# Optimization experiments

Measured on AMD Instinct MI355X. Metric: run time of the kernel, lower is better.

The kernel has to match this reference:

```python
import jax, jax.numpy as jnp
import numpy as np

N, E, G, F = 100000, 3200000, 256, 15
NEG_SLOPE = 0.2


def _lin(k, fi, fo):
    s = 1.0 / np.sqrt(fi)
    return jax.random.uniform(k, (fi, fo), jnp.float32, -s, s)


def _vec(k, n, fi):
    s = 1.0 / np.sqrt(fi)
    return jax.random.uniform(k, (n,), jnp.float32, -s, s)


def setup_inputs() -> dict:
    key = jax.random.key(0)
    ks = jax.random.split(key, 40)
    inp = {}
    inp["x"] = jax.random.normal(ks[0], (N, F), jnp.float32)
    inp["edge_index"] = jax.random.randint(ks[1], (2, E), 0, N, dtype=jnp.int32)
    inp["batch"] = jnp.sort(jax.random.randint(ks[2], (N,), 0, G, dtype=jnp.int32))
    inp["xA"] = jax.random.normal(ks[3], (G, 300), jnp.float32)
    i = 4
    for l in (1, 2, 3):
        inp[f"cW{l}"] = _lin(ks[i], F, F); i += 1
        inp[f"cas{l}"] = _vec(ks[i], F, F); i += 1
        inp[f"cad{l}"] = _vec(ks[i], F, F); i += 1
        inp[f"cb{l}"] = jnp.zeros((F,), jnp.float32)
        inp[f"fW{l}"] = _lin(ks[i], F, F); i += 1
        inp[f"fb{l}"] = _vec(ks[i], F, F); i += 1
    inp["m1W"] = _lin(ks[i], 90, 90); i += 1
    inp["m1b"] = _vec(ks[i], 90, 90); i += 1
    inp["aW1"] = _lin(ks[i], 300, 300); i += 1
    inp["ab1"] = _vec(ks[i], 300, 300); i += 1
    inp["aW2"] = _lin(ks[i], 300, 300); i += 1
    inp["ab2"] = _vec(ks[i], 300, 300); i += 1
    inp["aW3"] = _lin(ks[i], 300, 300); i += 1
    inp["ab3"] = _vec(ks[i], 300, 300); i += 1
    inp["aW4"] = _lin(ks[i], 300, 45); i += 1
    inp["ab4"] = _vec(ks[i], 45, 300); i += 1
    inp["m2W"] = _lin(ks[i], 90, 1); i += 1
    inp["m2b"] = _vec(ks[i], 1, 90); i += 1
    return inp


def _gat(x, src, dst, W, a_s, a_d, b):
    """PyG GATConv (heads=1, add_self_loops handled by caller via src/dst)."""
    h = x @ W                                        # [N, F]
    e = jax.nn.leaky_relu((h @ a_s)[src] + (h @ a_d)[dst], NEG_SLOPE)  # [E+N]
    mx = jax.ops.segment_max(e, dst, num_segments=N)
    ex = jnp.exp(e - mx[dst])
    den = jax.ops.segment_sum(ex, dst, num_segments=N)
    alpha = ex / (den[dst] + 1e-16)                   # segment softmax over dst
    out = jax.ops.segment_sum(h[src] * alpha[:, None], dst, num_segments=N)
    return out + b


def reference(x, edge_index, batch, xA,
              cW1, cas1, cad1, cb1, fW1, fb1,
              cW2, cas2, cad2, cb2, fW2, fb2,
              cW3, cas3, cad3, cb3, fW3, fb3,
              m1W, m1b, aW1, ab1, aW2, ab2, aW3, ab3, aW4, ab4,
              m2W, m2b):
    loop = jnp.arange(N, dtype=edge_index.dtype)      # self loops
    src = jnp.concatenate([edge_index[0], loop])
    dst = jnp.concatenate([edge_index[1], loop])

    h = _gat(x, src, dst, cW1, cas1, cad1, cb1)
    h = jax.nn.relu(h @ fW1 + fb1)
    h = _gat(h, src, dst, cW2, cas2, cad2, cb2)
    h = jax.nn.relu(h @ fW2 + fb2)
    h = _gat(h, src, dst, cW3, cas3, cad3, cb3)
    h = h @ fW3 + fb3

    s = jax.ops.segment_sum(h, batch, num_segments=G)
    mx = jax.ops.segment_max(h, batch, num_segments=G)
    cnt = jax.ops.segment_sum(jnp.ones((N, 1), h.dtype), batch, num_segments=G)
    mean = s / jnp.maximum(cnt, 1.0)
    pooled = jnp.concatenate([s, mx, mean], axis=1)   # [G, 45]

    a = jax.nn.relu(xA @ aW1 + ab1)
    a = jax.nn.relu(a @ aW2 + ab2)
    a = jax.nn.sigmoid(a @ aW3 + ab3)
    xann = a @ aW4 + ab4                              # [G, 45]

    z = jnp.concatenate([pooled, xann], axis=1)       # [G, 90]
    z = jax.nn.relu(z @ m1W + m1b)
    z = z @ m2W + m2b
    return jax.nn.sigmoid(z)
```

## Files before the change

### kernel.cpp

```cpp
#include <hip/hip_runtime.h>
#include <hip/hip_bf16.h>
#include <math.h>

#define FDIM 15
#define FPAD 16
#define NEG_SLOPE 0.2f
#define BSH 8
#define BWID 256
#define HB_GRID 256
#define HB_BLK 1024

typedef _Float16 half_t;

__device__ __forceinline__ float leaky(float e) {
  return fmaxf(NEG_SLOPE * e, e);
}

__global__ void k_zero(int* __restrict__ p, int n) {
  int i = blockIdx.x * blockDim.x + threadIdx.x;
  if (i < n) p[i] = 0;
}

__global__ void k_bhist(const int* __restrict__ dstI, int* __restrict__ bcnt,
                        int n_tot, int n_real, int NB) {
  __shared__ int hist[512];
  int tid = threadIdx.x;
  for (int i = tid; i < NB; i += blockDim.x) hist[i] = 0;
  __syncthreads();
  int stride = gridDim.x * blockDim.x;
  for (int i = blockIdx.x * blockDim.x + tid; i < n_tot; i += stride) {
    int d = (i < n_real) ? dstI[i] : (i - n_real);
    atomicAdd(&hist[d >> BSH], 1);
  }
  __syncthreads();
  for (int i = tid; i < NB; i += blockDim.x)
    if (hist[i]) atomicAdd(&bcnt[i], hist[i]);
}

__global__ void k_bscan(const int* __restrict__ bcnt, int* __restrict__ boff,
                        int* __restrict__ bcur, int* __restrict__ rowptr,
                        int NB, int N, int total) {
  __shared__ int s[512];
  int tid = threadIdx.x;
  int v = (tid < NB) ? bcnt[tid] : 0;
  s[tid] = v;
  __syncthreads();
  for (int off = 1; off < 512; off <<= 1) {
    int add = (tid >= off) ? s[tid - off] : 0;
    __syncthreads();
    s[tid] += add;
    __syncthreads();
  }
  if (tid < NB) { int e = s[tid] - v; boff[tid] = e; bcur[tid] = e; }
  if (tid == NB - 1) boff[NB] = s[tid];
  if (tid == 0) rowptr[N] = total;
}

__global__ void k_bpart(const int* __restrict__ srcI, const int* __restrict__ dstI,
                        int* __restrict__ bcur, int* __restrict__ bbuf,
                        int n_tot, int n_real, int NB) {
  __shared__ int hist[512];
  __shared__ int base[512];
  int tid = threadIdx.x;
  for (int i = tid; i < NB; i += blockDim.x) hist[i] = 0;
  __syncthreads();
  int stride = gridDim.x * blockDim.x;
  int g0 = blockIdx.x * blockDim.x + tid;
  for (int i = g0; i < n_tot; i += stride) {
    int d = (i < n_real) ? dstI[i] : (i - n_real);
    atomicAdd(&hist[d >> BSH], 1);
  }
  __syncthreads();
  for (int i = tid; i < NB; i += blockDim.x)
    base[i] = hist[i] ? atomicAdd(&bcur[i], hist[i]) : 0;
  __syncthreads();
  for (int i = tid; i < NB; i += blockDim.x) hist[i] = 0;
  __syncthreads();
  for (int i = g0; i < n_tot; i += stride) {
    int s, d;
    if (i < n_real) { s = srcI[i]; d = dstI[i]; }
    else { s = d = i - n_real; }
    int b = d >> BSH;
    int p = base[b] + atomicAdd(&hist[b], 1);
    bbuf[p] = (s << BSH) | (d & (BWID - 1));
  }
}

__global__ void k_bbuild(const int* __restrict__ boff, const int* __restrict__ bbuf,
                         int* __restrict__ rowptr, int* __restrict__ csr, int N) {
  __shared__ int hist[BWID];
  __shared__ int sc[BWID];
  int b = blockIdx.x;
  int tid = threadIdx.x;
  int base_dst = b << BSH;
  int nd = min(BWID, N - base_dst);
  int s0 = boff[b], s1 = boff[b + 1];
  if (tid < BWID) hist[tid] = 0;
  __syncthreads();
  for (int j = s0 + tid; j < s1; j += 512)
    atomicAdd(&hist[bbuf[j] & (BWID - 1)], 1);
  __syncthreads();
  int v = 0;
  if (tid < BWID) { v = hist[tid]; sc[tid] = v; }
  __syncthreads();
  for (int off = 1; off < BWID; off <<= 1) {
    int add = 0;
    if (tid < BWID && tid >= off) add = sc[tid - off];
    __syncthreads();
    if (tid < BWID) sc[tid] += add;
    __syncthreads();
  }
  if (tid < nd) rowptr[base_dst + tid] = s0 + sc[tid] - v;
  __syncthreads();
  if (tid < BWID) hist[tid] = sc[tid] - v;
  __syncthreads();
  for (int j = s0 + tid; j < s1; j += 512) {
    int e = bbuf[j];
    int dl = e & (BWID - 1);
    int p = s0 + atomicAdd(&hist[dl], 1);
    csr[p] = (e >> BSH) << 5;
  }
}

__global__ void k_transform(const float* __restrict__ in, int ld_in,
                            const float* __restrict__ W,
                            const float* __restrict__ a_s,
                            const float* __restrict__ a_d,
                            half_t* __restrict__ hp,
                            float* __restrict__ ad_,
                            int n_nodes) {
  __shared__ float Ws[FDIM * FDIM];
  __shared__ float asv[FDIM], adv[FDIM];
  int tid = threadIdx.x;
  if (tid < FDIM * FDIM) Ws[tid] = W[tid];
  if (tid < FDIM) { asv[tid] = a_s[tid]; adv[tid] = a_d[tid]; }
  __syncthreads();
  int n = blockIdx.x * blockDim.x + tid;
  if (n >= n_nodes) return;
  float xin[FDIM];
#pragma unroll
  for (int j = 0; j < FDIM; ++j) xin[j] = in[n * ld_in + j];
  float sa = 0.f, da = 0.f;
  half_t hrow[FPAD];
#pragma unroll
  for (int o = 0; o < FDIM; ++o) {
    float acc = 0.f;
#pragma unroll
    for (int k = 0; k < FDIM; ++k) acc += xin[k] * Ws[k * FDIM + o];
    hrow[o] = (half_t)acc;
    sa += acc * asv[o];
    da += acc * adv[o];
  }
  hrow[FDIM] = (half_t)sa;
  ad_[n] = da;
  float4 w0, w1;
  __builtin_memcpy(&w0, &hrow[0], 16);
  __builtin_memcpy(&w1, &hrow[8], 16);
  float4* dst = (float4*)(hp + (size_t)n * FPAD);
  dst[0] = w0;
  dst[1] = w1;
}

__device__ __forceinline__ void mlp_rider(int g, int tid, int nthreads,
                                          const float* __restrict__ mIn,
                                          const float* __restrict__ mW,
                                          const float* __restrict__ mB,
                                          float* __restrict__ mOut,
                                          int Nout, int mAct,
                                          float* mins) {
  for (int k = tid; k < 300; k += nthreads) mins[k] = mIn[(size_t)g * 300 + k];
  __syncthreads();
  int j1 = tid;
  int j2 = tid + nthreads;
  bool p1 = (j1 < Nout), p2 = (j2 < Nout);
  if (!p1) return;
  float a0 = 0.f, a1 = 0.f, a2 = 0.f, a3 = 0.f;
  float a4 = 0.f, a5 = 0.f, a6 = 0.f, a7 = 0.f;
  float b0 = 0.f, b1 = 0.f, b2 = 0.f, b3 = 0.f;
  float b4 = 0.f, b5 = 0.f, b6 = 0.f, b7 = 0.f;
  int k = 0;
  for (; k + 7 < 300; k += 8) {
    float i0 = mins[k],     i1 = mins[k + 1], i2 = mins[k + 2], i3 = mins[k + 3];
    float i4 = mins[k + 4], i5 = mins[k + 5], i6 = mins[k + 6], i7 = mins[k + 7];
    float w0 = mW[k * Nout + j1];
    float w1 = mW[(k + 1) * Nout + j1];
    float w2 = mW[(k + 2) * Nout + j1];
    float w3 = mW[(k + 3) * Nout + j1];
    float w4 = mW[(k + 4) * Nout + j1];
    float w5 = mW[(k + 5) * Nout + j1];
    float w6 = mW[(k + 6) * Nout + j1];
    float w7 = mW[(k + 7) * Nout + j1];
    a0 += i0 * w0; a1 += i1 * w1; a2 += i2 * w2; a3 += i3 * w3;
    a4 += i4 * w4; a5 += i5 * w5; a6 += i6 * w6; a7 += i7 * w7;
    if (p2) {
      float v0 = mW[k * Nout + j2];
      float v1 = mW[(k + 1) * Nout + j2];
      float v2 = mW[(k + 2) * Nout + j2];
      float v3 = mW[(k + 3) * Nout + j2];
      float v4 = mW[(k + 4) * Nout + j2];
      float v5 = mW[(k + 5) * Nout + j2];
      float v6 = mW[(k + 6) * Nout + j2];
      float v7 = mW[(k + 7) * Nout + j2];
      b0 += i0 * v0; b1 += i1 * v1; b2 += i2 * v2; b3 += i3 * v3;
      b4 += i4 * v4; b5 += i5 * v5; b6 += i6 * v6; b7 += i7 * v7;
    }
  }
  for (; k < 300; ++k) {
    float ik = mins[k];
    a0 += ik * mW[k * Nout + j1];
    if (p2) b0 += ik * mW[k * Nout + j2];
  }
  float r1 = mB[j1] + ((a0 + a1) + (a2 + a3)) + ((a4 + a5) + (a6 + a7));
  if (mAct == 1) r1 = fmaxf(r1, 0.f);
  else if (mAct == 2) r1 = 1.f / (1.f + expf(-r1));
  mOut[(size_t)g * Nout + j1] = r1;
  if (p2) {
    float r2 = mB[j2] + ((b0 + b1) + (b2 + b3)) + ((b4 + b5) + (b6 + b7));
    if (mAct == 1) r2 = fmaxf(r2, 0.f);
    else if (mAct == 2) r2 = 1.f / (1.f + expf(-r2));
    mOut[(size_t)g * Nout + j2] = r2;
  }
}

__global__ void k_gat(const int* __restrict__ rowptr, const int* __restrict__ csrB,
                      const half_t* __restrict__ hp, const float* __restrict__ ad_,
                      const float* __restrict__ cb, const float* __restrict__ fW,
                      const float* __restrict__ fb,
                      const float* __restrict__ nW, const float* __restrict__ nas,
                      const float* __restrict__ nad,
                      half_t* __restrict__ hp2, float* __restrict__ ad2,
                      float* __restrict__ fout,
                      const float* __restrict__ mIn, const float* __restrict__ mW,
                      const float* __restrict__ mB, float* __restrict__ mOut,
                      int mNout, int mAct, int mlpG,
                      int n_nodes, int do_relu, int fuse) {
  __shared__ float Ws[FDIM * FDIM];
  __shared__ float W2s[FDIM * FDIM];
  __shared__ float cbv[FDIM], fbv[FDIM], as2v[FDIM], ad2v[FDIM];
  __shared__ float aggT[16][16];
  __shared__ float outT[16][16];
  __shared__ float mins[304];
  int tid = threadIdx.x;

  if ((int)blockIdx.x < mlpG) {
    mlp_rider(blockIdx.x, tid, blockDim.x, mIn, mW, mB, mOut, mNout, mAct, mins);
    return;
  }

  if (tid < FDIM * FDIM) Ws[tid] = fW[tid];
  if (tid < FDIM) { cbv[tid] = cb[tid]; fbv[tid] = fb[tid]; }
  if (fuse) {
    if (tid < FDIM * FDIM) W2s[tid] = nW[tid];
    if (tid < FDIM) { as2v[tid] = nas[tid]; ad2v[tid] = nad[tid]; }
  }
  __syncthreads();
  int dl = tid >> 4;
  int f  = tid & 15;
  int d  = ((int)blockIdx.x - mlpG) * 16 + dl;
  float val = 0.f;
  if (d < n_nodes) {
    int rs = rowptr[d], re = rowptr[d + 1];
    float adv = ad_[d];
    const char* hb = (const char*)hp;
    int fo = f << 1;
    float den0 = 0.f, acc0 = 0.f, den1 = 0.f, acc1 = 0.f;
    int j = rs;
    for (; j + 7 < re; j += 8) {
      int o0 = csrB[j],     o1 = csrB[j + 1], o2 = csrB[j + 2], o3 = csrB[j + 3];
      int o4 = csrB[j + 4], o5 = csrB[j + 5], o6 = csrB[j + 6], o7 = csrB[j + 7];
      float hv0 = (float)*(const half_t*)(hb + o0 + fo);
      float hv1 = (float)*(const half_t*)(hb + o1 + fo);
      float hv2 = (float)*(const half_t*)(hb + o2 + fo);
      float hv3 = (float)*(const half_t*)(hb + o3 + fo);
      float hv4 = (float)*(const half_t*)(hb + o4 + fo);
      float hv5 = (float)*(const half_t*)(hb + o5 + fo);
      float hv6 = (float)*(const half_t*)(hb + o6 + fo);
      float hv7 = (float)*(const half_t*)(hb + o7 + fo);
      float w0 = __expf(leaky(__shfl(hv0, 15, 16) + adv));
      float w1 = __expf(leaky(__shfl(hv1, 15, 16) + adv));
      float w2 = __expf(leaky(__shfl(hv2, 15, 16) + adv));
      float w3 = __expf(leaky(__shfl(hv3, 15, 16) + adv));
      float w4 = __expf(leaky(__shfl(hv4, 15, 16) + adv));
      float w5 = __expf(leaky(__shfl(hv5, 15, 16) + adv));
      float w6 = __expf(leaky(__shfl(hv6, 15, 16) + adv));
      float w7 = __expf(leaky(__shfl(hv7, 15, 16) + adv));
      den0 += w0; acc0 += hv0 * w0;
      den1 += w1; acc1 += hv1 * w1;
      den0 += w2; acc0 += hv2 * w2;
      den1 += w3; acc1 += hv3 * w3;
      den0 += w4; acc0 += hv4 * w4;
      den1 += w5; acc1 += hv5 * w5;
      den0 += w6; acc0 += hv6 * w6;
      den1 += w7; acc1 += hv7 * w7;
    }
    for (; j < re; ++j) {
      int o0 = csrB[j];
      float hv0 = (float)*(const half_t*)(hb + o0 + fo);
      float w0 = __expf(leaky(__shfl(hv0, 15, 16) + adv));
      den0 += w0; acc0 += hv0 * w0;
    }
    val = (acc0 + acc1) / (den0 + den1 + 1e-16f);
  }
  aggT[dl][f] = (f < FDIM) ? (val + cbv[f]) : 0.f;
  __syncthreads();
  int o = f;
  float ffn = 0.f;
  if (o < FDIM) {
    ffn = fbv[o];
#pragma unroll
    for (int k = 0; k < FDIM; ++k) ffn += aggT[dl][k] * Ws[k * FDIM + o];
    if (do_relu) ffn = fmaxf(ffn, 0.f);
  }
  if (!fuse) {
    if (d < n_nodes) fout[d * FPAD + o] = (o < FDIM) ? ffn : 0.f;
    return;
  }
  outT[dl][o] = ffn;
  __syncthreads();
  if (d < n_nodes) {
    float h2 = 0.f;
    if (o < FDIM) {
#pragma unroll
      for (int k = 0; k < FDIM; ++k) h2 += outT[dl][k] * W2s[k * FDIM + o];
    }
    float pa = (o < FDIM) ? h2 * as2v[o] : 0.f;
    float pd = (o < FDIM) ? h2 * ad2v[o] : 0.f;
#pragma unroll
    for (int k = 8; k; k >>= 1) {
      pa += __shfl_xor(pa, k, 16);
      pd += __shfl_xor(pd, k, 16);
    }
    hp2[(size_t)d * FPAD + o] = (half_t)((o < FDIM) ? h2 : pa);
    if (o == 0) ad2[d] = pd;
  }
}

__device__ __forceinline__ int lowerb(const int* __restrict__ a, int n, int key) {
  int lo = 0, hi = n;
  while (lo < hi) { int mid = (lo + hi) >> 1; if (a[mid] < key) lo = mid + 1; else hi = mid; }
  return lo;
}

__global__ void k_pool(const float* __restrict__ fout, const int* __restrict__ batch,
                       float* __restrict__ pooled,
                       const float* __restrict__ acts,
                       const float* __restrict__ aW4, const float* __restrict__ ab4,
                       float* __restrict__ xann,
                       int n_nodes, int Gn) {
  __shared__ float ss[256], sm[256];
  __shared__ float mins[304];
  int tid = threadIdx.x;
  if ((int)blockIdx.x < Gn) {
    mlp_rider(blockIdx.x, tid, blockDim.x, acts, aW4, ab4, xann, 45, 0, mins);
    return;
  }
  int g = blockIdx.x - Gn;
  int s = lowerb(batch, n_nodes, g);
  int e = lowerb(batch, n_nodes, g + 1);
  int f = tid & 15;
  float sum = 0.f, mx = -INFINITY;
  for (int n = s + (tid >> 4); n < e; n += 16) {
    float v = fout[n * FPAD + f];
    sum += v;
    mx = fmaxf(mx, v);
  }
  ss[tid] = sum; sm[tid] = mx;
  __syncthreads();
  for (int step = 128; step >= 16; step >>= 1) {
    if (tid < step) { ss[tid] += ss[tid + step]; sm[tid] = fmaxf(sm[tid], sm[tid + step]); }
    __syncthreads();
  }
  if (tid < FDIM) {
    float cnt = (float)(e - s);
    float sv = ss[tid];
    pooled[g * 45 + tid] = sv;
    pooled[g * 45 + 15 + tid] = sm[tid];
    pooled[g * 45 + 30 + tid] = sv / fmaxf(cnt, 1.f);
  }
}

__global__ void k_final(const float* __restrict__ pooled, const float* __restrict__ xann,
                        const float* __restrict__ m1W, const float* __restrict__ m1b,
                        const float* __restrict__ m2W, const float* __restrict__ m2b,
                        float* __restrict__ out) {
  __shared__ float z[90];
  __shared__ float z2[90];
  __shared__ float ps[128];
  int g = blockIdx.x;
  int t = threadIdx.x;
  if (t < 45) z[t] = pooled[g * 45 + t];
  else if (t < 90) z[t] = xann[g * 45 + (t - 45)];
  __syncthreads();
  if (t < 90) {
    float a0 = 0.f, a1 = 0.f;
    for (int k = 0; k < 90; k += 2) {
      float w0 = m1W[k * 90 + t];
      float w1 = m1W[(k + 1) * 90 + t];
      a0 += z[k] * w0; a1 += z[k + 1] * w1;
    }
    z2[t] = fmaxf(m1b[t] + a0 + a1, 0.f);
  }
  __syncthreads();
  if (t < 90) ps[t] = z2[t] * m2W[t];
  else ps[t] = 0.f;
  __syncthreads();
  if (t < 64) {
    float v = ps[t] + ps[t + 64];
#pragma unroll
    for (int k2 = 32; k2; k2 >>= 1) v += __shfl_xor(v, k2, 64);
    if (t == 0) out[g] = 1.f / (1.f + expf(-(v + m2b[0])));
  }
}

extern "C" void kernel_launch(void* const* d_in, const int* in_sizes, int n_in,
                              void* d_out, int out_size, void* d_ws, size_t ws_size,
                              hipStream_t stream) {
  const float* x   = (const float*)d_in[0];
  const int* ei    = (const int*)d_in[1];
  const int* batch = (const int*)d_in[2];
  const float* xA  = (const float*)d_in[3];

  const int N = in_sizes[0] / FDIM;
  const int E = in_sizes[1] / 2;
  const int G = in_sizes[3] / 300;
  const int ET = E + N;
  const int NB = (N + BWID - 1) >> BSH;

  const int* srcI = ei;
  const int* dstI = ei + E;

  float* ws = (float*)d_ws;
  size_t layerW = (size_t)34 * N;
  size_t uSize = layerW > (size_t)ET ? layerW : (size_t)ET;
  size_t off = 0;
  int*    bbuf = (int*)(ws + off);
  half_t* hpA  = (half_t*)(ws + off);
  half_t* hpB  = (half_t*)(ws + off + (size_t)8 * N);
  float*  adA  = ws + off + (size_t)16 * N;
  float*  adB  = ws + off + (size_t)17 * N;
  float*  fout = ws + off + (size_t)18 * N;
  off += uSize;
  int*   rowptr = (int*)(ws + off); off += N + 1;
  int*   csr    = (int*)(ws + off); off += (size_t)ET;
  int*   bcnt   = (int*)(ws + off); off += 516;
  int*   boff   = (int*)(ws + off); off += 516;
  int*   bcur   = (int*)(ws + off); off += 516;
  float* pooled = ws + off; off += (size_t)G * 45;
  float* a1     = ws + off; off += (size_t)G * 300;
  float* a2     = ws + off; off += (size_t)G * 300;
  float* xann   = ws + off; off += (size_t)G * 45;

  const int B = 256;
  const int gN = (N + B - 1) / B;

  k_zero<<<(NB + B - 1) / B, B, 0, stream>>>(bcnt, NB);
  k_bhist<<<HB_GRID, HB_BLK, 0, stream>>>(dstI, bcnt, ET, E, NB);
  k_bscan<<<1, 512, 0, stream>>>(bcnt, boff, bcur, rowptr, NB, N, ET);
  k_bpart<<<HB_GRID, HB_BLK, 0, stream>>>(srcI, dstI, bcur, bbuf, ET, E, NB);
  k_bbuild<<<NB, 512, 0, stream>>>(boff, bbuf, rowptr, csr, N);

  const float* cW1  = (const float*)d_in[4];
  const float* cas1 = (const float*)d_in[5];
  const float* cad1 = (const float*)d_in[6];
  const float* cb1  = (const float*)d_in[7];
  const float* fW1  = (const float*)d_in[8];
  const float* fb1  = (const float*)d_in[9];
  const float* cW2  = (const float*)d_in[10];
  const float* cas2 = (const float*)d_in[11];
  const float* cad2 = (const float*)d_in[12];
  const float* cb2  = (const float*)d_in[13];
  const float* fW2  = (const float*)d_in[14];
  const float* fb2  = (const float*)d_in[15];
  const float* cW3  = (const float*)d_in[16];
  const float* cas3 = (const float*)d_in[17];
  const float* cad3 = (const float*)d_in[18];
  const float* cb3  = (const float*)d_in[19];
  const float* fW3  = (const float*)d_in[20];
  const float* fb3  = (const float*)d_in[21];
  const float* m1W  = (const float*)d_in[22];
  const float* m1b  = (const float*)d_in[23];
  const float* aW1  = (const float*)d_in[24];
  const float* ab1  = (const float*)d_in[25];
  const float* aW2  = (const float*)d_in[26];
  const float* ab2  = (const float*)d_in[27];
  const float* aW3  = (const float*)d_in[28];
  const float* ab3  = (const float*)d_in[29];
  const float* aW4  = (const float*)d_in[30];
  const float* ab4  = (const float*)d_in[31];
  const float* m2W  = (const float*)d_in[32];
  const float* m2b  = (const float*)d_in[33];

  const int gGat = (N + 15) / 16;
  k_transform<<<gN, B, 0, stream>>>(x, FDIM, cW1, cas1, cad1, hpA, adA, N);
  k_gat<<<gGat + G, B, 0, stream>>>(rowptr, csr, hpA, adA, cb1, fW1, fb1,
                                    cW2, cas2, cad2, hpB, adB, nullptr,
                                    xA, aW1, ab1, a1, 300, 1, G,
                                    N, 1, 1);
  k_gat<<<gGat + G, B, 0, stream>>>(rowptr, csr, hpB, adB, cb2, fW2, fb2,
                                    cW3, cas3, cad3, hpA, adA, nullptr,
                                    a1, aW2, ab2, a2, 300, 1, G,
                                    N, 1, 1);
  k_gat<<<gGat + G, B, 0, stream>>>(rowptr, csr, hpA, adA, cb3, fW3, fb3,
                                    nullptr, nullptr, nullptr, nullptr, nullptr, fout,
                                    a2, aW3, ab3, a1, 300, 2, G,
                                    N, 0, 0);

  k_pool<<<2 * G, B, 0, stream>>>(fout, batch, pooled, a1, aW4, ab4, xann, N, G);

  k_final<<<G, 128, 0, stream>>>(pooled, xann, m1W, m1b, m2W, m2b, (float*)d_out);
}
```

Measured before the change: 356.3 us.

## Fuse layer-1 transform into histogram kernel and replace global atomics with per-block hists

The first-layer node transform now runs inside the destination-bucket histogram kernel as extra blocks, saving one launch and letting the two jobs run concurrently. Each histogram block now writes its private counts to a per-block array, and the scan kernel sums them. This removes the zeroing kernel and the global atomics. Workspace buffers are no longer aliased, since the transform output would otherwise overlap bbuf, and the layout grows by one edge-sized region plus the per-block histogram area. The scan now reads 256x512 ints on a single block, which adds serial latency there.

New measurement: 361.0 us. No clear change (+1.3%).

```diff
diff --git a/kernel.cpp b/kernel.cpp
--- a/kernel.cpp
+++ b/kernel.cpp
@@ -16,33 +16,83 @@
   return fmaxf(NEG_SLOPE * e, e);
 }
 
-__global__ void k_zero(int* __restrict__ p, int n) {
-  int i = blockIdx.x * blockDim.x + threadIdx.x;
-  if (i < n) p[i] = 0;
-}
-
-__global__ void k_bhist(const int* __restrict__ dstI, int* __restrict__ bcnt,
-                        int n_tot, int n_real, int NB) {
+__global__ void k_bh_tr(const int* __restrict__ dstI, int* __restrict__ hists,
+                        int n_tot, int n_real, int NB,
+                        const float* __restrict__ in,
+                        const float* __restrict__ W,
+                        const float* __restrict__ a_s,
+                        const float* __restrict__ a_d,
+                        half_t* __restrict__ hp, float* __restrict__ ad_,
+                        int n_nodes) {
   __shared__ int hist[512];
+  __shared__ float Ws[FDIM * FDIM];
+  __shared__ float asv[FDIM], adv[FDIM];
   int tid = threadIdx.x;
-  for (int i = tid; i < NB; i += blockDim.x) hist[i] = 0;
-  __syncthreads();
-  int stride = gridDim.x * blockDim.x;
-  for (int i = blockIdx.x * blockDim.x + tid; i < n_tot; i += stride) {
-    int d = (i < n_real) ? dstI[i] : (i - n_real);
-    atomicAdd(&hist[d >> BSH], 1);
-  }
-  __syncthreads();
-  for (int i = tid; i < NB; i += blockDim.x)
-    if (hist[i]) atomicAdd(&bcnt[i], hist[i]);
-}
-
-__global__ void k_bscan(const int* __restrict__ bcnt, int* __restrict__ boff,
+  if ((int)blockIdx.x < HB_GRID) {
+    for (int i = tid; i < NB; i += blockDim.x) hist[i] = 0;
+    __syncthreads();
+    int stride = HB_GRID * blockDim.x;
+    for (int i = blockIdx.x * blockDim.x + tid; i < n_tot; i += stride) {
+      int d = (i < n_real) ? dstI[i] : (i - n_real);
+      atomicAdd(&hist[d >> BSH], 1);
+    }
+    __syncthreads();
+    for (int i = tid; i < NB; i += blockDim.x)
+      hists[blockIdx.x * 512 + i] = hist[i];
+    return;
+  }
+  int bid = blockIdx.x - HB_GRID;
+  if (tid < FDIM * FDIM) Ws[tid] = W[tid];
+  if (tid < FDIM) { asv[tid] = a_s[tid]; adv[tid] = a_d[tid]; }
+  __syncthreads();
+  int n = bid * blockDim.x + tid;
+  if (n >= n_nodes) return;
+  float xin[FDIM];
+#pragma unroll
+  for (int j = 0; j < FDIM; ++j) xin[j] = in[n * FDIM + j];
+  float sa = 0.f, da = 0.f;
+  half_t hrow[FPAD];
+#pragma unroll
+  for (int o = 0; o < FDIM; ++o) {
+    float acc = 0.f;
+#pragma unroll
+    for (int k = 0; k < FDIM; ++k) acc += xin[k] * Ws[k * FDIM + o];
+    hrow[o] = (half_t)acc;
+    sa += acc * asv[o];
+    da += acc * adv[o];
+  }
+  hrow[FDIM] = (half_t)sa;
+  ad_[n] = da;
+  float4 w0, w1;
+  __builtin_memcpy(&w0, &hrow[0], 16);
+  __builtin_memcpy(&w1, &hrow[8], 16);
+  float4* dst = (float4*)(hp + (size_t)n * FPAD);
+  dst[0] = w0;
+  dst[1] = w1;
+}
+
+__global__ void k_bscan(const int* __restrict__ hists, int* __restrict__ boff,
                         int* __restrict__ bcur, int* __restrict__ rowptr,
                         int NB, int N, int total) {
   __shared__ int s[512];
   int tid = threadIdx.x;
-  int v = (tid < NB) ? bcnt[tid] : 0;
+  int v = 0;
+  if (tid < NB) {
+    int a0 = 0, a1 = 0, a2 = 0, a3 = 0, a4 = 0, a5 = 0, a6 = 0, a7 = 0;
+    int blk = 0;
+    for (; blk + 7 < HB_GRID; blk += 8) {
+      a0 += hists[(blk + 0) * 512 + tid];
+      a1 += hists[(blk + 1) * 512 + tid];
+      a2 += hists[(blk + 2) * 512 + tid];
+      a3 += hists[(blk + 3) * 512 + tid];
+      a4 += hists[(blk + 4) * 512 + tid];
+      a5 += hists[(blk + 5) * 512 + tid];
+      a6 += hists[(blk + 6) * 512 + tid];
+      a7 += hists[(blk + 7) * 512 + tid];
+    }
+    for (; blk < HB_GRID; ++blk) a0 += hists[blk * 512 + tid];
+    v = ((a0 + a1) + (a2 + a3)) + ((a4 + a5) + (a6 + a7));
+  }
   s[tid] = v;
   __syncthreads();
   for (int off = 1; off < 512; off <<= 1) {
@@ -120,45 +170,6 @@
     int p = s0 + atomicAdd(&hist[dl], 1);
     csr[p] = (e >> BSH) << 5;
   }
-}
-
-__global__ void k_transform(const float* __restrict__ in, int ld_in,
-                            const float* __restrict__ W,
-                            const float* __restrict__ a_s,
-                            const float* __restrict__ a_d,
-                            half_t* __restrict__ hp,
-                            float* __restrict__ ad_,
-                            int n_nodes) {
-  __shared__ float Ws[FDIM * FDIM];
-  __shared__ float asv[FDIM], adv[FDIM];
-  int tid = threadIdx.x;
-  if (tid < FDIM * FDIM) Ws[tid] = W[tid];
-  if (tid < FDIM) { asv[tid] = a_s[tid]; adv[tid] = a_d[tid]; }
-  __syncthreads();
-  int n = blockIdx.x * blockDim.x + tid;
-  if (n >= n_nodes) return;
-  float xin[FDIM];
-#pragma unroll
-  for (int j = 0; j < FDIM; ++j) xin[j] = in[n * ld_in + j];
-  float sa = 0.f, da = 0.f;
-  half_t hrow[FPAD];
-#pragma unroll
-  for (int o = 0; o < FDIM; ++o) {
-    float acc = 0.f;
-#pragma unroll
-    for (int k = 0; k < FDIM; ++k) acc += xin[k] * Ws[k * FDIM + o];
-    hrow[o] = (half_t)acc;
-    sa += acc * asv[o];
-    da += acc * adv[o];
-  }
-  hrow[FDIM] = (half_t)sa;
-  ad_[n] = da;
-  float4 w0, w1;
-  __builtin_memcpy(&w0, &hrow[0], 16);
-  __builtin_memcpy(&w1, &hrow[8], 16);
-  float4* dst = (float4*)(hp + (size_t)n * FPAD);
-  dst[0] = w0;
-  dst[1] = w1;
 }
 
 __device__ __forceinline__ void mlp_rider(int g, int tid, int nthreads,
@@ -430,19 +441,16 @@
   const int* dstI = ei + E;
 
   float* ws = (float*)d_ws;
-  size_t layerW = (size_t)34 * N;
-  size_t uSize = layerW > (size_t)ET ? layerW : (size_t)ET;
   size_t off = 0;
-  int*    bbuf = (int*)(ws + off);
-  half_t* hpA  = (half_t*)(ws + off);
-  half_t* hpB  = (half_t*)(ws + off + (size_t)8 * N);
-  float*  adA  = ws + off + (size_t)16 * N;
-  float*  adB  = ws + off + (size_t)17 * N;
-  float*  fout = ws + off + (size_t)18 * N;
-  off += uSize;
+  half_t* hpA  = (half_t*)(ws + off); off += (size_t)8 * N;
+  half_t* hpB  = (half_t*)(ws + off); off += (size_t)8 * N;
+  float*  adA  = ws + off; off += N;
+  float*  adB  = ws + off; off += N;
+  float*  fout = ws + off; off += (size_t)16 * N;
+  int*    bbuf = (int*)(ws + off); off += (size_t)ET;
   int*   rowptr = (int*)(ws + off); off += N + 1;
   int*   csr    = (int*)(ws + off); off += (size_t)ET;
-  int*   bcnt   = (int*)(ws + off); off += 516;
+  int*   hists  = (int*)(ws + off); off += (size_t)HB_GRID * 512;
   int*   boff   = (int*)(ws + off); off += 516;
   int*   bcur   = (int*)(ws + off); off += 516;
   float* pooled = ws + off; off += (size_t)G * 45;
@@ -451,13 +459,6 @@
   float* xann   = ws + off; off += (size_t)G * 45;
 
   const int B = 256;
-  const int gN = (N + B - 1) / B;
-
-  k_zero<<<(NB + B - 1) / B, B, 0, stream>>>(bcnt, NB);
-  k_bhist<<<HB_GRID, HB_BLK, 0, stream>>>(dstI, bcnt, ET, E, NB);
-  k_bscan<<<1, 512, 0, stream>>>(bcnt, boff, bcur, rowptr, NB, N, ET);
-  k_bpart<<<HB_GRID, HB_BLK, 0, stream>>>(srcI, dstI, bcur, bbuf, ET, E, NB);
-  k_bbuild<<<NB, 512, 0, stream>>>(boff, bbuf, rowptr, csr, N);
 
   const float* cW1  = (const float*)d_in[4];
   const float* cas1 = (const float*)d_in[5];
@@ -490,8 +491,14 @@
   const float* m2W  = (const float*)d_in[32];
   const float* m2b  = (const float*)d_in[33];
 
+  const int gTr = (N + HB_BLK - 1) / HB_BLK;
+  k_bh_tr<<<HB_GRID + gTr, HB_BLK, 0, stream>>>(dstI, hists, ET, E, NB,
+                                                x, cW1, cas1, cad1, hpA, adA, N);
+  k_bscan<<<1, 512, 0, stream>>>(hists, boff, bcur, rowptr, NB, N, ET);
+  k_bpart<<<HB_GRID, HB_BLK, 0, stream>>>(srcI, dstI, bcur, bbuf, ET, E, NB);
+  k_bbuild<<<NB, 512, 0, stream>>>(boff, bbuf, rowptr, csr, N);
+
   const int gGat = (N + 15) / 16;
-  k_transform<<<gN, B, 0, stream>>>(x, FDIM, cW1, cas1, cad1, hpA, adA, N);
   k_gat<<<gGat + G, B, 0, stream>>>(rowptr, csr, hpA, adA, cb1, fW1, fb1,
                                     cW2, cas2, cad2, hpB, adB, nullptr,
                                     xA, aW1, ab1, a1, 300, 1, G,
```
